# Kernel optimization log

Measured on AMD Instinct MI355X. Metric: run time of the kernel, lower is better.

Reference implementation:

```python
import jax, jax.numpy as jnp
import numpy as np

N_NODES = 100000
IN_DIM = 64
OUT_DIM = 64
N_EDGES = 1600000


def _undirected_self_loops(edge_index, num_nodes):
    """Symmetrize, add self loops, coalesce (dedup+sort) like the torch module.
    edge_index is an integer constant, so we preprocess with numpy (no grads flow here).
    Returns (src, dst, w) where w are symmetric GCN normalization weights.
    """
    ei = np.asarray(edge_index, dtype=np.int64)
    loops = np.arange(num_nodes, dtype=np.int64)
    full_src = np.concatenate([ei[0], ei[1], loops])
    full_dst = np.concatenate([ei[1], ei[0], loops])
    keys = np.unique(full_src * num_nodes + full_dst)  # coalesce, sorted
    src = keys // num_nodes
    dst = keys % num_nodes
    deg = np.bincount(dst, minlength=num_nodes).clip(min=1)
    inv_sqrt = deg.astype(np.float32) ** -0.5
    w = inv_sqrt[src] * inv_sqrt[dst]
    return src, dst, w


def setup_inputs() -> dict:
    key = jax.random.key(0)
    kx, kw, kb, ke = jax.random.split(key, 4)
    x = jax.random.normal(kx, (N_NODES, IN_DIM), dtype=jnp.float32)
    # nn.Linear params: W (out, in), b (out,)
    W = jax.random.normal(kw, (OUT_DIM, IN_DIM), dtype=jnp.float32) / np.sqrt(IN_DIM)
    b = jax.random.normal(kb, (OUT_DIM,), dtype=jnp.float32) * 0.01
    edge_index = jax.random.randint(ke, (2, N_EDGES), 0, N_NODES, dtype=jnp.int64)
    return {"x": x, "edge_index": edge_index, "W": W, "b": b}


def reference(x, edge_index, W, b) -> jnp.ndarray:
    n = x.shape[0]
    src_np, dst_np, w_np = _undirected_self_loops(edge_index, n)
    src = jnp.asarray(src_np)
    dst = jnp.asarray(dst_np)
    w = jnp.asarray(w_np).astype(x.dtype)  # (E',)
    h = x @ W.T + b                         # (N, out_dim)
    msg = h[src] * w[:, None]               # gather + per-edge scale, (E', out_dim)
    out = jnp.zeros_like(h).at[dst].add(msg)  # scatter-add aggregation
    return out
```

## Files before the change

### kernel.cpp

```cpp
#include <hip/hip_runtime.h>
#include <hip/hip_bf16.h>
#include <stdint.h>

#define NN 100000
#define EE 1600000
#define CAP 80
#define NB 782
#define CAPB 5120
#define HTS 8192
#define EMPTY 0xFFFFFFFFu
#define BCH 4096
#define GBIN 391
#define GLIN 1563

typedef float fx2 __attribute__((ext_vector_type(2)));

__device__ __forceinline__ unsigned int mix32(unsigned int x){
  x ^= x >> 16; x *= 0x7feb352du;
  x ^= x >> 15; x *= 0x846ca68bu;
  x ^= x >> 16;
  return x;
}

extern "C" __global__ __launch_bounds__(256)
void k_prep(const float* __restrict__ x, const float* __restrict__ W,
            const float* __restrict__ bias, __hip_bfloat16* __restrict__ hb,
            const int* __restrict__ ei, int* __restrict__ bcnt,
            unsigned int* __restrict__ bbuf){
  __shared__ __align__(16) char sm[17920];
  const int tid = threadIdx.x;
  const int bid = blockIdx.x;
  const bool isbin = (bid < GBIN);
  const int sub = isbin ? bid : (bid - GBIN);

  if (!isbin){
    __hip_bfloat16 (*wt)[72] = reinterpret_cast<__hip_bfloat16(*)[72]>(sm);
    __hip_bfloat16 (*xs)[68] = reinterpret_cast<__hip_bfloat16(*)[68]>(sm + 9216);
    const int lane = tid & 63;
    const int wv   = tid >> 6;
    #pragma unroll
    for (int r = 0; r < 16; ++r){
      int i = r*4 + wv;
      wt[i][lane] = __float2bfloat16(W[lane*64 + i]);
    }
    const int nbase = sub * 64;
    #pragma unroll
    for (int r = 0; r < 4; ++r){
      int idx = r*256 + tid;
      int nl  = idx >> 4;
      int c4  = idx & 15;
      int n   = nbase + nl;
      float4 v = make_float4(0.f,0.f,0.f,0.f);
      if (n < NN) v = reinterpret_cast<const float4*>(x)[(size_t)n*16 + c4];
      xs[c4*4+0][nl] = __float2bfloat16(v.x);
      xs[c4*4+1][nl] = __float2bfloat16(v.y);
      xs[c4*4+2][nl] = __float2bfloat16(v.z);
      xs[c4*4+3][nl] = __float2bfloat16(v.w);
    }
    __syncthreads();

    const int og  = tid & 7;
    const int nl0 = (tid >> 3) * 2;
    float acc[2][8];
    #pragma unroll
    for (int t=0;t<2;++t){
      #pragma unroll
      for (int j=0;j<8;++j) acc[t][j]=0.f;
    }
    #pragma unroll 4
    for (int i=0;i<64;++i){
      uint4 wq = *reinterpret_cast<const uint4*>(&wt[i][og*8]);
      float w0 = __uint_as_float(wq.x << 16), w1 = __uint_as_float(wq.x & 0xFFFF0000u);
      float w2 = __uint_as_float(wq.y << 16), w3 = __uint_as_float(wq.y & 0xFFFF0000u);
      float w4 = __uint_as_float(wq.z << 16), w5 = __uint_as_float(wq.z & 0xFFFF0000u);
      float w6 = __uint_as_float(wq.w << 16), w7 = __uint_as_float(wq.w & 0xFFFF0000u);
      unsigned xv = *reinterpret_cast<const unsigned*>(&xs[i][nl0]);
      float x0 = __uint_as_float(xv << 16);
      float x1 = __uint_as_float(xv & 0xFFFF0000u);
      acc[0][0] += x0*w0; acc[0][1] += x0*w1; acc[0][2] += x0*w2; acc[0][3] += x0*w3;
      acc[0][4] += x0*w4; acc[0][5] += x0*w5; acc[0][6] += x0*w6; acc[0][7] += x0*w7;
      acc[1][0] += x1*w0; acc[1][1] += x1*w1; acc[1][2] += x1*w2; acc[1][3] += x1*w3;
      acc[1][4] += x1*w4; acc[1][5] += x1*w5; acc[1][6] += x1*w6; acc[1][7] += x1*w7;
    }
    float4 b0 = reinterpret_cast<const float4*>(bias)[og*2];
    float4 b1 = reinterpret_cast<const float4*>(bias)[og*2+1];
    float bb[8] = {b0.x,b0.y,b0.z,b0.w,b1.x,b1.y,b1.z,b1.w};
    #pragma unroll
    for (int t=0;t<2;++t){
      int n = nbase + nl0 + t;
      if (n < NN){
        union { uint4 u4; __hip_bfloat16 v[8]; } pk;
        #pragma unroll
        for (int j=0;j<8;++j) pk.v[j] = __float2bfloat16(acc[t][j] + bb[j]);
        reinterpret_cast<uint4*>(&hb[(size_t)n*64])[og] = pk.u4;
      }
    }
  } else {
    int* hist  = reinterpret_cast<int*>(sm);
    int* bbase = hist + NB;
    int* bcur  = bbase + NB;
    for (int i = tid; i < NB; i += 256) hist[i] = 0;
    __syncthreads();
    const int base4 = sub * 1024;
    const int4* ea4 = reinterpret_cast<const int4*>(ei);
    const int4* ec4 = reinterpret_cast<const int4*>(ei + EE);
    int4 A[4], C[4];
    #pragma unroll
    for (int r = 0; r < 4; ++r){
      int idx = base4 + r*256 + tid;
      if (idx < (EE >> 2)){
        A[r] = ea4[idx]; C[r] = ec4[idx];
        atomicAdd(&hist[C[r].x >> 7], 1); atomicAdd(&hist[A[r].x >> 7], 1);
        atomicAdd(&hist[C[r].y >> 7], 1); atomicAdd(&hist[A[r].y >> 7], 1);
        atomicAdd(&hist[C[r].z >> 7], 1); atomicAdd(&hist[A[r].z >> 7], 1);
        atomicAdd(&hist[C[r].w >> 7], 1); atomicAdd(&hist[A[r].w >> 7], 1);
      } else A[r].x = -1;
    }
    __syncthreads();
    for (int bk = tid; bk < NB; bk += 256){
      int hh = hist[bk];
      bbase[bk] = hh ? atomicAdd(&bcnt[bk], hh) : 0;
      bcur[bk]  = 0;
    }
    __syncthreads();
    #pragma unroll
    for (int r = 0; r < 4; ++r){
      if (A[r].x >= 0){
#define PLACE(a,c) { \
        int b1 = (c) >> 7, b2 = (a) >> 7; \
        int p1 = bbase[b1] + atomicAdd(&bcur[b1], 1); \
        int p2 = bbase[b2] + atomicAdd(&bcur[b2], 1); \
        if (p1 < CAPB) bbuf[(size_t)b1*CAPB + p1] = ((unsigned)(a) << 7) | (unsigned)((c) & 127); \
        if (p2 < CAPB) bbuf[(size_t)b2*CAPB + p2] = ((unsigned)(c) << 7) | (unsigned)((a) & 127); }
        PLACE(A[r].x, C[r].x) PLACE(A[r].y, C[r].y)
        PLACE(A[r].z, C[r].z) PLACE(A[r].w, C[r].w)
#undef PLACE
      }
    }
  }
}

extern "C" __global__ __launch_bounds__(256)
void k_dedup(const int* __restrict__ bcnt, const unsigned int* __restrict__ bbuf,
             unsigned int* __restrict__ srclist, int* __restrict__ cnt,
             float* __restrict__ inv){
  __shared__ unsigned int HT[HTS];
  __shared__ int dcur[128];
  const int tid = threadIdx.x;
  const int b   = blockIdx.x;
  const int d0  = b << 7;
  uint4* HT4 = reinterpret_cast<uint4*>(HT);
  #pragma unroll
  for (int r = 0; r < 8; ++r) HT4[r*256 + tid] = make_uint4(EMPTY,EMPTY,EMPTY,EMPTY);
  if (tid < 128) dcur[tid] = 0;
  __syncthreads();

  int n = bcnt[b]; if (n > CAPB) n = CAPB;
  const unsigned int* buf = bbuf + (size_t)b * CAPB;
  for (int k = tid; k < n; k += 256){
    unsigned int pk  = buf[k];
    unsigned int idx = mix32(pk) & (HTS-1);
    for (;;){
      unsigned int prev = atomicCAS(&HT[idx], EMPTY, pk);
      if (prev == EMPTY || prev == pk) break;
      idx = (idx + 1) & (HTS-1);
    }
  }
  if (tid < 128 && d0 + tid < NN){
    unsigned int pk  = ((unsigned)(d0 + tid) << 7) | (unsigned)tid;
    unsigned int idx = mix32(pk) & (HTS-1);
    for (;;){
      unsigned int prev = atomicCAS(&HT[idx], EMPTY, pk);
      if (prev == EMPTY || prev == pk) break;
      idx = (idx + 1) & (HTS-1);
    }
  }
  __syncthreads();

  for (int i = tid; i < HTS; i += 256){
    unsigned int v = HT[i];
    if (v != EMPTY){
      int dl  = v & 127;
      int pos = atomicAdd(&dcur[dl], 1);
      if (pos < CAP) srclist[(size_t)(d0 + dl) * CAP + pos] = v >> 7;
    }
  }
  __syncthreads();
  if (tid < 128 && d0 + tid < NN){
    int c = dcur[tid];
    cnt[d0 + tid] = c;
    inv[d0 + tid] = rsqrtf((float)c);
  }
}

extern "C" __global__ __launch_bounds__(256)
void k_agg(const __hip_bfloat16* __restrict__ hb, const float* __restrict__ inv,
           const int* __restrict__ cnt, const unsigned int* __restrict__ srclist,
           float* __restrict__ out){
  __shared__ uint2 sv[4][CAP];
  const int wv   = threadIdx.x >> 6;
  const int lane = threadIdx.x & 63;
  const int half = lane >> 5;
  const int pl   = lane & 31;
  const int d    = blockIdx.x*4 + wv;
  if (d >= NN) return;
  const unsigned int* reg = srclist + (size_t)d * CAP;
  int c = cnt[d]; if (c > CAP) c = CAP;
  const int c16 = (c + 15) & ~15;

  if (lane < c){
    unsigned s = __builtin_nontemporal_load(reg + lane);
    sv[wv][lane] = make_uint2(s, __float_as_uint(inv[s]));
  }
  if (64 + lane < c){
    unsigned s = __builtin_nontemporal_load(reg + 64 + lane);
    sv[wv][64 + lane] = make_uint2(s, __float_as_uint(inv[s]));
  }
  { int p = c + lane; if (p < c16) sv[wv][p] = make_uint2(0u, 0u); }

  const char* hbase = (const char*)hb;
  const int   boff  = pl << 2;
  float ax[8], ay[8];
  #pragma unroll
  for (int u=0;u<8;++u){ ax[u]=0.f; ay[u]=0.f; }
  #pragma unroll 1
  for (int j = 0; j < c16; j += 16){
    #pragma unroll
    for (int u = 0; u < 8; ++u){
      uint2 e = sv[wv][j + 2*u + half];
      float w = __uint_as_float(e.y);
      unsigned hv = *reinterpret_cast<const unsigned*>(hbase + ((size_t)e.x << 7) + boff);
      ax[u] += w * __uint_as_float(hv << 16);
      ay[u] += w * __uint_as_float(hv & 0xFFFF0000u);
    }
  }
  float rx = ((ax[0]+ax[1])+(ax[2]+ax[3])) + ((ax[4]+ax[5])+(ax[6]+ax[7]));
  float ry = ((ay[0]+ay[1])+(ay[2]+ay[3])) + ((ay[4]+ay[5])+(ay[6]+ay[7]));
  rx += __shfl_xor(rx, 32);
  ry += __shfl_xor(ry, 32);
  if (half == 0){
    float iv = inv[d];
    fx2 o; o.x = rx * iv; o.y = ry * iv;
    __builtin_nontemporal_store(o, reinterpret_cast<fx2*>(&out[(size_t)d*64 + (pl << 1)]));
  }
}

extern "C" void kernel_launch(void* const* d_in, const int* in_sizes, int n_in,
                              void* d_out, int out_size, void* d_ws, size_t ws_size,
                              hipStream_t stream){
  (void)in_sizes; (void)n_in; (void)out_size; (void)ws_size;
  const float* x  = (const float*)d_in[0];
  const int*   ei = (const int*)  d_in[1];
  const float* W  = (const float*)d_in[2];
  const float* b  = (const float*)d_in[3];
  float* out = (float*)d_out;

  char* ws = (char*)d_ws;
  __hip_bfloat16* hb      = (__hip_bfloat16*)ws;
  float*          inv     = (float*)(ws + 12800000);
  int*            cnt     = (int*)  (ws + 13200000);
  unsigned int*   srclist = (unsigned int*)(ws + 13600000);
  int*            bcnt    = (int*)  (ws + 45600000);
  unsigned int*   bbuf    = (unsigned int*)(ws + 45604096);

  (void)hipMemsetAsync(bcnt, 0, NB * 4, stream);

  k_prep  <<<GBIN + GLIN, 256, 0, stream>>>(x, W, b, hb, ei, bcnt, bbuf);
  k_dedup <<<NB, 256, 0, stream>>>(bcnt, bbuf, srclist, cnt, inv);
  k_agg   <<<(NN + 3)/4, 256, 0, stream>>>(hb, inv, cnt, srclist, out);
}
```

Baseline: 148.3 us.

## Slice bf16 features into four 16-column planes and aggregate per slice

```diff
diff --git a/kernel.cpp b/kernel.cpp
--- a/kernel.cpp
+++ b/kernel.cpp
@@ -9,9 +9,9 @@
 #define CAPB 5120
 #define HTS 8192
 #define EMPTY 0xFFFFFFFFu
-#define BCH 4096
 #define GBIN 391
 #define GLIN 1563
+#define SLN (NN*16)
 
 typedef float fx2 __attribute__((ext_vector_type(2)));
 
@@ -24,7 +24,7 @@
 
 extern "C" __global__ __launch_bounds__(256)
 void k_prep(const float* __restrict__ x, const float* __restrict__ W,
-            const float* __restrict__ bias, __hip_bfloat16* __restrict__ hb,
+            const float* __restrict__ bias, __hip_bfloat16* __restrict__ hs,
             const int* __restrict__ ei, int* __restrict__ bcnt,
             unsigned int* __restrict__ bbuf){
   __shared__ __align__(16) char sm[17920];
@@ -85,6 +85,7 @@
     float4 b0 = reinterpret_cast<const float4*>(bias)[og*2];
     float4 b1 = reinterpret_cast<const float4*>(bias)[og*2+1];
     float bb[8] = {b0.x,b0.y,b0.z,b0.w,b1.x,b1.y,b1.z,b1.w};
+    const int sl = og >> 1, hf = og & 1;
     #pragma unroll
     for (int t=0;t<2;++t){
       int n = nbase + nl0 + t;
@@ -92,7 +93,7 @@
         union { uint4 u4; __hip_bfloat16 v[8]; } pk;
         #pragma unroll
         for (int j=0;j<8;++j) pk.v[j] = __float2bfloat16(acc[t][j] + bb[j]);
-        reinterpret_cast<uint4*>(&hb[(size_t)n*64])[og] = pk.u4;
+        reinterpret_cast<uint4*>(hs)[(size_t)sl*(SLN>>3) + n*2 + hf] = pk.u4;
       }
     }
   } else {
@@ -194,54 +195,55 @@
 }
 
 extern "C" __global__ __launch_bounds__(256)
-void k_agg(const __hip_bfloat16* __restrict__ hb, const float* __restrict__ inv,
+void k_agg(const __hip_bfloat16* __restrict__ hs, const float* __restrict__ inv,
            const int* __restrict__ cnt, const unsigned int* __restrict__ srclist,
            float* __restrict__ out){
   __shared__ uint2 sv[4][CAP];
   const int wv   = threadIdx.x >> 6;
   const int lane = threadIdx.x & 63;
-  const int half = lane >> 5;
-  const int pl   = lane & 31;
-  const int d    = blockIdx.x*4 + wv;
+  const int eg   = lane >> 3;
+  const int pl   = lane & 7;
+  const int bid  = blockIdx.x;
+  const int rr   = bid & 7;
+  const int s    = rr >> 1;
+  const int d    = ((bid >> 3)*2 + (rr & 1))*4 + wv;
   if (d >= NN) return;
   const unsigned int* reg = srclist + (size_t)d * CAP;
   int c = cnt[d]; if (c > CAP) c = CAP;
   const int c16 = (c + 15) & ~15;
 
   if (lane < c){
-    unsigned s = __builtin_nontemporal_load(reg + lane);
-    sv[wv][lane] = make_uint2(s, __float_as_uint(inv[s]));
+    unsigned sS = __builtin_nontemporal_load(reg + lane);
+    sv[wv][lane] = make_uint2(sS, __float_as_uint(inv[sS]));
   }
   if (64 + lane < c){
-    unsigned s = __builtin_nontemporal_load(reg + 64 + lane);
-    sv[wv][64 + lane] = make_uint2(s, __float_as_uint(inv[s]));
+    unsigned sS = __builtin_nontemporal_load(reg + 64 + lane);
+    sv[wv][64 + lane] = make_uint2(sS, __float_as_uint(inv[sS]));
   }
   { int p = c + lane; if (p < c16) sv[wv][p] = make_uint2(0u, 0u); }
 
-  const char* hbase = (const char*)hb;
-  const int   boff  = pl << 2;
-  float ax[8], ay[8];
-  #pragma unroll
-  for (int u=0;u<8;++u){ ax[u]=0.f; ay[u]=0.f; }
+  const char* hbase = (const char*)(hs + (size_t)s * SLN);
+  float ax0 = 0.f, ay0 = 0.f, ax1 = 0.f, ay1 = 0.f;
   #pragma unroll 1
   for (int j = 0; j < c16; j += 16){
-    #pragma unroll
-    for (int u = 0; u < 8; ++u){
-      uint2 e = sv[wv][j + 2*u + half];
-      float w = __uint_as_float(e.y);
-      unsigned hv = *reinterpret_cast<const unsigned*>(hbase + ((size_t)e.x << 7) + boff);
-      ax[u] += w * __uint_as_float(hv << 16);
-      ay[u] += w * __uint_as_float(hv & 0xFFFF0000u);
-    }
-  }
-  float rx = ((ax[0]+ax[1])+(ax[2]+ax[3])) + ((ax[4]+ax[5])+(ax[6]+ax[7]));
-  float ry = ((ay[0]+ay[1])+(ay[2]+ay[3])) + ((ay[4]+ay[5])+(ay[6]+ay[7]));
-  rx += __shfl_xor(rx, 32);
-  ry += __shfl_xor(ry, 32);
-  if (half == 0){
+    uint2 e0 = sv[wv][j + eg];
+    uint2 e1 = sv[wv][j + 8 + eg];
+    unsigned h0 = *reinterpret_cast<const unsigned*>(hbase + ((size_t)e0.x << 5) + (pl << 2));
+    unsigned h1 = *reinterpret_cast<const unsigned*>(hbase + ((size_t)e1.x << 5) + (pl << 2));
+    float w0 = __uint_as_float(e0.y), w1 = __uint_as_float(e1.y);
+    ax0 += w0 * __uint_as_float(h0 << 16);
+    ay0 += w0 * __uint_as_float(h0 & 0xFFFF0000u);
+    ax1 += w1 * __uint_as_float(h1 << 16);
+    ay1 += w1 * __uint_as_float(h1 & 0xFFFF0000u);
+  }
+  float rx = ax0 + ax1, ry = ay0 + ay1;
+  rx += __shfl_xor(rx, 8);  ry += __shfl_xor(ry, 8);
+  rx += __shfl_xor(rx, 16); ry += __shfl_xor(ry, 16);
+  rx += __shfl_xor(rx, 32); ry += __shfl_xor(ry, 32);
+  if (eg == 0){
     float iv = inv[d];
     fx2 o; o.x = rx * iv; o.y = ry * iv;
-    __builtin_nontemporal_store(o, reinterpret_cast<fx2*>(&out[(size_t)d*64 + (pl << 1)]));
+    __builtin_nontemporal_store(o, reinterpret_cast<fx2*>(&out[(size_t)d*64 + s*16 + (pl << 1)]));
   }
 }
 
@@ -256,7 +258,7 @@
   float* out = (float*)d_out;
 
   char* ws = (char*)d_ws;
-  __hip_bfloat16* hb      = (__hip_bfloat16*)ws;
+  __hip_bfloat16* hs      = (__hip_bfloat16*)ws;
   float*          inv     = (float*)(ws + 12800000);
   int*            cnt     = (int*)  (ws + 13200000);
   unsigned int*   srclist = (unsigned int*)(ws + 13600000);
@@ -265,7 +267,7 @@
 
   (void)hipMemsetAsync(bcnt, 0, NB * 4, stream);
 
-  k_prep  <<<GBIN + GLIN, 256, 0, stream>>>(x, W, b, hb, ei, bcnt, bbuf);
+  k_prep  <<<GBIN + GLIN, 256, 0, stream>>>(x, W, b, hs, ei, bcnt, bbuf);
   k_dedup <<<NB, 256, 0, stream>>>(bcnt, bbuf, srclist, cnt, inv);
-  k_agg   <<<(NN + 3)/4, 256, 0, stream>>>(hb, inv, cnt, srclist, out);
-}
+  k_agg   <<<100000, 256, 0, stream>>>(hs, inv, cnt, srclist, out);
+}
```

Measured after the change: 255.0 us. +72.0%, slower.
